# Kernel tuning notes

Hardware: AMD Instinct MI355X
Metric: run time of the kernel (lower is better)

Reference implementation:

```python
import jax, jax.numpy as jnp
import numpy as np

HEADS = 8
DIM_HEAD = 64
LN_EPS = 1e-5


def _layernorm(x, gamma, beta):
    mu = jnp.mean(x, axis=-1, keepdims=True)
    var = jnp.var(x, axis=-1, keepdims=True)
    return (x - mu) * jax.lax.rsqrt(var + LN_EPS) * gamma + beta


def setup_inputs() -> dict:
    key = jax.random.key(0)
    ks = jax.random.split(key, 5)
    B, N, D = 1, 16384, 512
    return {
        "x": jax.random.normal(ks[0], (B, N, D), dtype=jnp.float32),
        "ln_gamma": jnp.ones((D,), dtype=jnp.float32),
        "ln_beta": jnp.zeros((D,), dtype=jnp.float32),
        "w_qkv": jax.random.normal(ks[1], (D, 3 * D), dtype=jnp.float32) * (D ** -0.5),
        "agent": jax.random.normal(ks[2], (HEADS, 512, DIM_HEAD), dtype=jnp.float32) * (DIM_HEAD ** -0.5),
        "w_out": jax.random.normal(ks[3], (D, D), dtype=jnp.float32) * (D ** -0.5),
        "b_out": jnp.zeros((D,), dtype=jnp.float32),
    }


def reference(x, ln_gamma, ln_beta, w_qkv, agent, w_out, b_out):
    # TransLayer: x + Mask_Agent_Attention(LayerNorm(x))
    B, N, D = x.shape
    xn = _layernorm(x, ln_gamma, ln_beta)

    qkv = xn @ w_qkv                                   # [B, N, 3D]
    q, k, v = jnp.split(qkv, 3, axis=-1)
    # [B, H, N, d]
    q = q.reshape(B, N, HEADS, DIM_HEAD).transpose(0, 2, 1, 3)
    k = k.reshape(B, N, HEADS, DIM_HEAD).transpose(0, 2, 1, 3)
    v = v.reshape(B, N, HEADS, DIM_HEAD).transpose(0, 2, 1, 3)

    scale = DIM_HEAD ** -0.5  # tem=0 -> classical 1/sqrt(d) scaling

    # agents aggregate values: softmax over keys  [B, H, A, N]
    attn1 = jax.nn.softmax(jnp.einsum('had,bhnd->bhan', agent, k) * scale, axis=-1)
    agent_v = jnp.einsum('bhan,bhnd->bhad', attn1, v)  # [B, H, A, d]

    # queries attend to agents: softmax over agents  [B, H, N, A]
    attn2 = jax.nn.softmax(jnp.einsum('bhnd,had->bhna', q, agent) * scale, axis=-1)
    out = jnp.einsum('bhna,bhad->bhnd', attn2, agent_v)  # [B, H, N, d]

    out = out + v  # residual=True: value residual inside attention
    out = out.transpose(0, 2, 1, 3).reshape(B, N, D)
    out = out @ w_out + b_out
    return x + out
```

## Files before the change

### kernel.cpp

```cpp
#include <hip/hip_runtime.h>
#include <stdint.h>

typedef unsigned short u16;
typedef __attribute__((ext_vector_type(8))) short bf16x8;
typedef __attribute__((ext_vector_type(4))) float f32x4;

__device__ __forceinline__ float bf2f(u16 u){
  union { uint32_t i; float f; } v; v.i = ((uint32_t)u) << 16; return v.f;
}
__device__ __forceinline__ u16 f2bf(float f){
  union { float fl; uint32_t i; } v; v.fl = f;
  uint32_t r = v.i + 0x7FFFu + ((v.i >> 16) & 1u);
  return (u16)(r >> 16);
}
__device__ __forceinline__ f32x4 mfma16(bf16x8 a, bf16x8 b, f32x4 c){
  return __builtin_amdgcn_mfma_f32_16x16x32_bf16(a, b, c, 0, 0, 0);
}

__global__ __launch_bounds__(256) void k_conv_bf(const float* __restrict__ in, u16* __restrict__ out, int n){
  int i = (blockIdx.x * 256 + threadIdx.x) * 4;
  if (i >= n) return;
  float4 v = *(const float4*)(in + i);
  ushort4 o; o.x=f2bf(v.x); o.y=f2bf(v.y); o.z=f2bf(v.z); o.w=f2bf(v.w);
  *(ushort4*)(out + i) = o;
}

__global__ __launch_bounds__(256) void k_transp(const float* __restrict__ in, u16* __restrict__ out, int R, int C){
  __shared__ u16 tile[64][68];
  int c0 = blockIdx.x * 64, r0 = blockIdx.y * 64;
  int tr = threadIdx.x >> 4;
  int tc = (threadIdx.x & 15) * 4;
  for (int rr = 0; rr < 4; rr++){
    int r = rr * 16 + tr;
    float4 v = *(const float4*)(in + (size_t)(r0 + r) * C + c0 + tc);
    ushort4 o; o.x=f2bf(v.x); o.y=f2bf(v.y); o.z=f2bf(v.z); o.w=f2bf(v.w);
    *(ushort4*)&tile[r][tc] = o;
  }
  __syncthreads();
  for (int rr = 0; rr < 4; rr++){
    int oc = rr * 16 + tr;
    ushort4 o;
    o.x = tile[tc+0][oc]; o.y = tile[tc+1][oc]; o.z = tile[tc+2][oc]; o.w = tile[tc+3][oc];
    *(ushort4*)(out + (size_t)(c0 + oc) * R + r0 + tc) = o;
  }
}

__global__ __launch_bounds__(256) void k_transp_v(const u16* __restrict__ qkv, u16* __restrict__ vT){
  __shared__ u16 tile[64][68];
  int n0 = blockIdx.x * 64;
  int c0 = blockIdx.y * 64;
  int tr = threadIdx.x >> 4;
  int tc = (threadIdx.x & 15) * 4;
  for (int rr = 0; rr < 4; rr++){
    int r = rr * 16 + tr;
    ushort4 v = *(const ushort4*)(qkv + (size_t)(n0 + r) * 1536 + 1024 + c0 + tc);
    *(ushort4*)&tile[r][tc] = v;
  }
  __syncthreads();
  for (int rr = 0; rr < 4; rr++){
    int oc = rr * 16 + tr;
    ushort4 o;
    o.x = tile[tc+0][oc]; o.y = tile[tc+1][oc]; o.z = tile[tc+2][oc]; o.w = tile[tc+3][oc];
    *(ushort4*)(vT + (size_t)(c0 + oc) * 16384 + n0 + tc) = o;
  }
}

__global__ __launch_bounds__(128) void k_ln(const float* __restrict__ x, const float* __restrict__ g,
                                            const float* __restrict__ b, u16* __restrict__ xn){
  int row = blockIdx.x;
  int t = threadIdx.x;
  float4 v = *(const float4*)(x + (size_t)row * 512 + t * 4);
  float s = v.x + v.y + v.z + v.w;
  float q = v.x*v.x + v.y*v.y + v.z*v.z + v.w*v.w;
  for (int o = 32; o > 0; o >>= 1){ s += __shfl_down(s, o); q += __shfl_down(q, o); }
  __shared__ float red[4];
  if ((t & 63) == 0){ red[(t >> 6) * 2] = s; red[(t >> 6) * 2 + 1] = q; }
  __syncthreads();
  float mu  = (red[0] + red[2]) * (1.0f/512.0f);
  float var = (red[1] + red[3]) * (1.0f/512.0f) - mu * mu;
  float rs = rsqrtf(var + 1e-5f);
  float4 gv = *(const float4*)(g + t * 4);
  float4 bv = *(const float4*)(b + t * 4);
  ushort4 o;
  o.x = f2bf((v.x - mu) * rs * gv.x + bv.x);
  o.y = f2bf((v.y - mu) * rs * gv.y + bv.y);
  o.z = f2bf((v.z - mu) * rs * gv.z + bv.z);
  o.w = f2bf((v.w - mu) * rs * gv.w + bv.w);
  *(ushort4*)(xn + (size_t)row * 512 + t * 4) = o;
}

__global__ __launch_bounds__(256) void k_gemm_qkv(const u16* __restrict__ A, const u16* __restrict__ Bt,
                                                  u16* __restrict__ C){
  __shared__ u16 a_lds[128][72];
  __shared__ u16 b_lds[128][72];
  int m0 = blockIdx.x * 128, n0 = blockIdx.y * 128;
  int t = threadIdx.x, w = t >> 6, l = t & 63;
  int wm = (w >> 1) * 64, wn = (w & 1) * 64;
  f32x4 acc[4][4];
  for (int i=0;i<4;i++) for (int j=0;j<4;j++) acc[i][j] = {0.f,0.f,0.f,0.f};
  for (int k0 = 0; k0 < 512; k0 += 64){
    __syncthreads();
    for (int i = 0; i < 4; i++){
      int flat = t + 256 * i;
      int r = flat >> 3, c = (flat & 7) * 8;
      *(uint4*)&a_lds[r][c] = *(const uint4*)(A  + (size_t)(m0 + r) * 512 + k0 + c);
      *(uint4*)&b_lds[r][c] = *(const uint4*)(Bt + (size_t)(n0 + r) * 512 + k0 + c);
    }
    __syncthreads();
    for (int kk = 0; kk < 64; kk += 32){
      int kb = kk + (l >> 4) * 8;
      bf16x8 av[4], bv[4];
      for (int mt=0;mt<4;mt++) av[mt] = *(const bf16x8*)&a_lds[wm + mt*16 + (l & 15)][kb];
      for (int nt=0;nt<4;nt++) bv[nt] = *(const bf16x8*)&b_lds[wn + nt*16 + (l & 15)][kb];
      for (int mt=0;mt<4;mt++) for (int nt=0;nt<4;nt++)
        acc[mt][nt] = mfma16(av[mt], bv[nt], acc[mt][nt]);
    }
  }
  int rr = (l >> 4) * 4, cc = l & 15;
  for (int mt=0;mt<4;mt++) for (int nt=0;nt<4;nt++)
    for (int j=0;j<4;j++){
      int r = m0 + wm + mt*16 + rr + j;
      int c = n0 + wn + nt*16 + cc;
      C[(size_t)r * 1536 + c] = f2bf(acc[mt][nt][j]);
    }
}

__global__ __launch_bounds__(256) void k_gemm_out(const u16* __restrict__ A, const u16* __restrict__ Bt,
                                                  const float* __restrict__ x, const float* __restrict__ bias,
                                                  float* __restrict__ y){
  __shared__ u16 a_lds[128][72];
  __shared__ u16 b_lds[128][72];
  int m0 = blockIdx.x * 128, n0 = blockIdx.y * 128;
  int t = threadIdx.x, w = t >> 6, l = t & 63;
  int wm = (w >> 1) * 64, wn = (w & 1) * 64;
  f32x4 acc[4][4];
  for (int i=0;i<4;i++) for (int j=0;j<4;j++) acc[i][j] = {0.f,0.f,0.f,0.f};
  for (int k0 = 0; k0 < 512; k0 += 64){
    __syncthreads();
    for (int i = 0; i < 4; i++){
      int flat = t + 256 * i;
      int r = flat >> 3, c = (flat & 7) * 8;
      *(uint4*)&a_lds[r][c] = *(const uint4*)(A  + (size_t)(m0 + r) * 512 + k0 + c);
      *(uint4*)&b_lds[r][c] = *(const uint4*)(Bt + (size_t)(n0 + r) * 512 + k0 + c);
    }
    __syncthreads();
    for (int kk = 0; kk < 64; kk += 32){
      int kb = kk + (l >> 4) * 8;
      bf16x8 av[4], bv[4];
      for (int mt=0;mt<4;mt++) av[mt] = *(const bf16x8*)&a_lds[wm + mt*16 + (l & 15)][kb];
      for (int nt=0;nt<4;nt++) bv[nt] = *(const bf16x8*)&b_lds[wn + nt*16 + (l & 15)][kb];
      for (int mt=0;mt<4;mt++) for (int nt=0;nt<4;nt++)
        acc[mt][nt] = mfma16(av[mt], bv[nt], acc[mt][nt]);
    }
  }
  int rr = (l >> 4) * 4, cc = l & 15;
  for (int mt=0;mt<4;mt++) for (int nt=0;nt<4;nt++)
    for (int j=0;j<4;j++){
      int r = m0 + wm + mt*16 + rr + j;
      int c = n0 + wn + nt*16 + cc;
      y[(size_t)r * 512 + c] = acc[mt][nt][j] + bias[c] + x[(size_t)r * 512 + c];
    }
}

__global__ __launch_bounds__(256) void k_agent_agg(const u16* __restrict__ agbf, const u16* __restrict__ qkv,
                                                   const u16* __restrict__ vT,
                                                   float* __restrict__ nump, float* __restrict__ denp){
  int L = blockIdx.x;
  int g = (L >> 6) * 8 + (L & 7);
  int m = (L >> 3) & 7;
  int h = g >> 4, ch = g & 15, a0 = m * 64;

  __shared__ u16 ag[64][72];
  __shared__ u16 kt[64][72];
  __shared__ u16 vt[64][72];
  __shared__ u16 pt[64][72];
  int t = threadIdx.x, w = t >> 6, l = t & 63;

  for (int i = 0; i < 2; i++){
    int flat = t + 256 * i;
    int r = flat >> 3, c = (flat & 7) * 8;
    *(uint4*)&ag[r][c] = *(const uint4*)(agbf + (size_t)(h * 512 + a0 + r) * 64 + c);
  }

  bf16x8 ones;
  for (int i = 0; i < 8; i++) ones[i] = (short)0x3F80;

  f32x4 acc2[4];
  for (int i=0;i<4;i++) acc2[i] = {0.f,0.f,0.f,0.f};
  f32x4 accd = {0.f,0.f,0.f,0.f};

  for (int sub = 0; sub < 16; sub++){
    int n0 = ch * 1024 + sub * 64;
    __syncthreads();
    {
      int flat = t;
      int r = flat >> 3, c = (flat & 7) * 8;
      *(uint4*)&kt[r][c] = *(const uint4*)(qkv + (size_t)(n0 + r) * 1536 + 512 + h * 64 + c);
      int flat2 = t + 256;
      int r2 = flat2 >> 3, c2 = (flat2 & 7) * 8;
      *(uint4*)&kt[r2][c2] = *(const uint4*)(qkv + (size_t)(n0 + r2) * 1536 + 512 + h * 64 + c2);
      *(uint4*)&vt[r][c]   = *(const uint4*)(vT + ((size_t)(h * 64 + r) << 14) + n0 + c);
      *(uint4*)&vt[r2][c2] = *(const uint4*)(vT + ((size_t)(h * 64 + r2) << 14) + n0 + c2);
    }
    __syncthreads();

    f32x4 s[4];
    for (int nt=0;nt<4;nt++) s[nt] = {0.f,0.f,0.f,0.f};
    for (int kk = 0; kk < 64; kk += 32){
      int kb = kk + (l >> 4) * 8;
      bf16x8 kf = *(const bf16x8*)&kt[w*16 + (l & 15)][kb];
      for (int nt=0;nt<4;nt++){
        bf16x8 af = *(const bf16x8*)&ag[nt*16 + (l & 15)][kb];
        s[nt] = mfma16(kf, af, s[nt]);
      }
    }
    int nb = w*16 + (l >> 4) * 4;
    for (int nt=0;nt<4;nt++){
      int a = nt*16 + (l & 15);
      ushort4 o;
      o.x = f2bf(__expf(s[nt][0] * 0.125f));
      o.y = f2bf(__expf(s[nt][1] * 0.125f));
      o.z = f2bf(__expf(s[nt][2] * 0.125f));
      o.w = f2bf(__expf(s[nt][3] * 0.125f));
      *(ushort4*)&pt[a][nb] = o;
    }
    __syncthreads();

    for (int kk = 0; kk < 64; kk += 32){
      int kb = kk + (l >> 4) * 8;
      bf16x8 vf = *(const bf16x8*)&vt[w*16 + (l & 15)][kb];
      for (int mt=0;mt<4;mt++){
        bf16x8 pf = *(const bf16x8*)&pt[mt*16 + (l & 15)][kb];
        acc2[mt] = mfma16(pf, vf, acc2[mt]);
      }
      bf16x8 pw = *(const bf16x8*)&pt[w*16 + (l & 15)][kb];
      accd = mfma16(ones, pw, accd);
    }
  }

  size_t base = ((size_t)(h * 16 + ch) * 512 + a0) * 64;
  for (int mt=0;mt<4;mt++)
    #pragma unroll
    for (int j=0;j<4;j++){
      int a = mt*16 + (l>>4)*4 + j;
      int d = w*16 + (l&15);
      nump[base + (size_t)a*64 + d] = acc2[mt][j];
    }
  if (l < 16) denp[(size_t)(h*16 + ch) * 512 + a0 + w*16 + l] = accd[0];
}

__global__ __launch_bounds__(64) void k_agent_reduce(const float* __restrict__ nump, const float* __restrict__ denp,
                                                     u16* __restrict__ avtg){
  int h = blockIdx.x >> 9;
  int a = blockIdx.x & 511;
  int d = threadIdx.x;
  float num = 0.f, den = 0.f;
  for (int c = 0; c < 16; c++){
    num += nump[((size_t)(h * 16 + c) * 512 + a) * 64 + d];
    den += denp[(size_t)(h * 16 + c) * 512 + a];
  }
  avtg[((size_t)h * 64 + d) * 512 + a] = f2bf(num / den);
}

__global__ __launch_bounds__(256) void k_qattn(const u16* __restrict__ qkv, const u16* __restrict__ agbf,
                                               const u16* __restrict__ avtg, u16* __restrict__ atto){
  int n0 = blockIdx.x * 128;
  int h  = blockIdx.y;
  __shared__ u16 qt[128][72];
  __shared__ u16 avt[64][136];
  __shared__ u16 ubuf[128 * 136];
  __shared__ float dred[128][2];
  __shared__ float dnf[128];
  int t = threadIdx.x, w = t >> 6, l = t & 63;
  for (int i = 0; i < 4; i++){
    int flat = t + 256 * i;
    int r = flat >> 3, c = (flat & 7) * 8;
    *(uint4*)&qt[r][c] = *(const uint4*)(qkv + (size_t)(n0 + r) * 1536 + h * 64 + c);
  }
  f32x4 acc[4][2];
  for (int i=0;i<4;i++) for (int j=0;j<2;j++) acc[i][j] = {0.f,0.f,0.f,0.f};
  float dpart = 0.f;
  int wn = (w >> 1) * 64, wd = (w & 1) * 32, wa = (w & 1) * 64;
  for (int at = 0; at < 4; at++){
    int a0 = at * 128;
    __syncthreads();
    for (int i = 0; i < 4; i++){
      int flat = t + 256 * i;
      int r = flat >> 3, c = (flat & 7) * 8;
      *(uint4*)&ubuf[r * 72 + c] = *(const uint4*)(agbf + (size_t)(h * 512 + a0 + r) * 64 + c);
      int r2 = flat >> 4, c2 = (flat & 15) * 8;
      *(uint4*)&avt[r2][c2] = *(const uint4*)(avtg + (size_t)(h * 64 + r2) * 512 + a0 + c2);
    }
    __syncthreads();
    f32x4 s[4][4];
    for (int i=0;i<4;i++) for (int j=0;j<4;j++) s[i][j] = {0.f,0.f,0.f,0.f};
    for (int kk = 0; kk < 64; kk += 32){
      int kb = kk + (l >> 4) * 8;
      bf16x8 av[4], bv[4];
      for (int mt=0;mt<4;mt++) av[mt] = *(const bf16x8*)&qt[wn + mt*16 + (l&15)][kb];
      for (int nt=0;nt<4;nt++) bv[nt] = *(const bf16x8*)&ubuf[(size_t)(wa + nt*16 + (l&15)) * 72 + kb];
      for (int mt=0;mt<4;mt++) for (int nt=0;nt<4;nt++)
        s[mt][nt] = mfma16(av[mt], bv[nt], s[mt][nt]);
    }
    __syncthreads();
    for (int mt=0;mt<4;mt++) for (int nt=0;nt<4;nt++)
      #pragma unroll
      for (int j=0;j<4;j++){
        int n = wn + mt*16 + (l>>4)*4 + j;
        int a = wa + nt*16 + (l&15);
        ubuf[(size_t)n * 136 + a] = f2bf(__expf(s[mt][nt][j] * 0.125f));
      }
    __syncthreads();
    {
      const uint4* pp = (const uint4*)&ubuf[(size_t)(t >> 1) * 136 + (t & 1) * 64];
      float ds = 0.f;
      #pragma unroll
      for (int qq = 0; qq < 8; qq++){
        uint4 u = pp[qq];
        const u16* us = (const u16*)&u;
        for (int j=0;j<8;j++) ds += bf2f(us[j]);
      }
      dpart += ds;
    }
    for (int kk = 0; kk < 128; kk += 32){
      int kb = kk + (l >> 4) * 8;
      bf16x8 bv[2];
      for (int nt=0;nt<2;nt++) bv[nt] = *(const bf16x8*)&avt[wd + nt*16 + (l&15)][kb];
      for (int mt=0;mt<4;mt++){
        bf16x8 av = *(const bf16x8*)&ubuf[(size_t)(wn + mt*16 + (l&15)) * 136 + kb];
        for (int nt=0;nt<2;nt++)
          acc[mt][nt] = mfma16(av, bv[nt], acc[mt][nt]);
      }
    }
  }
  dred[t >> 1][t & 1] = dpart;
  __syncthreads();
  if (t < 128) dnf[t] = dred[t][0] + dred[t][1];
  __syncthreads();
  for (int mt=0;mt<4;mt++) for (int nt=0;nt<2;nt++)
    #pragma unroll
    for (int j=0;j<4;j++){
      int n = wn + mt*16 + (l>>4)*4 + j;
      int d = wd + nt*16 + (l&15);
      float v = bf2f(qkv[(size_t)(n0 + n) * 1536 + 1024 + h * 64 + d]);
      atto[(size_t)(n0 + n) * 512 + h * 64 + d] = f2bf(acc[mt][nt][j] / dnf[n] + v);
    }
}

extern "C" void kernel_launch(void* const* d_in, const int* in_sizes, int n_in,
                              void* d_out, int out_size, void* d_ws, size_t ws_size,
                              hipStream_t stream) {
  const float* x     = (const float*)d_in[0];
  const float* gamma = (const float*)d_in[1];
  const float* beta  = (const float*)d_in[2];
  const float* w_qkv = (const float*)d_in[3];
  const float* agent = (const float*)d_in[4];
  const float* w_out = (const float*)d_in[5];
  const float* b_out = (const float*)d_in[6];
  float* y = (float*)d_out;

  char* ws = (char*)d_ws;
  u16*   xn    = (u16*)  (ws + 0);
  u16*   vT    = (u16*)  (ws + 0);
  u16*   qkv   = (u16*)  (ws + 16777216);
  u16*   wqkvt = (u16*)  (ws + 67108864);
  u16*   woutt = (u16*)  (ws + 68681728);
  u16*   agbf  = (u16*)  (ws + 69206016);
  u16*   avtg  = (u16*)  (ws + 69730304);
  u16*   atto  = (u16*)  (ws + 70254592);
  float* nump  = (float*)(ws + 87031808);
  float* denp  = (float*)(ws + 103809024);

  k_conv_bf   <<<dim3(256),     dim3(256), 0, stream>>>(agent, agbf, 8*512*64);
  k_transp    <<<dim3(24, 8),   dim3(256), 0, stream>>>(w_qkv, wqkvt, 512, 1536);
  k_transp    <<<dim3(8, 8),    dim3(256), 0, stream>>>(w_out, woutt, 512, 512);
  k_ln        <<<dim3(16384),   dim3(128), 0, stream>>>(x, gamma, beta, xn);
  k_gemm_qkv  <<<dim3(128, 12), dim3(256), 0, stream>>>(xn, wqkvt, qkv);
  k_transp_v  <<<dim3(256, 8),  dim3(256), 0, stream>>>(qkv, vT);
  k_agent_agg <<<dim3(1024),    dim3(256), 0, stream>>>(agbf, qkv, vT, nump, denp);
  k_agent_reduce<<<dim3(4096),  dim3(64),  0, stream>>>(nump, denp, avtg);
  k_qattn     <<<dim3(128, 8),  dim3(256), 0, stream>>>(qkv, agbf, avtg, atto);
  k_gemm_out  <<<dim3(128, 4),  dim3(256), 0, stream>>>(atto, woutt, x, b_out, y);
}
```

Before: 187.4 us.

## Fold softmax scale into agents, use exp2, restructure query-attention tiling

Pre-scales the agent matrix by scale*log2(e) at conversion time so both softmax stages can use the hardware exp2 with no per-element multiply, and packs bf16 conversions with v_cvt_pk_bf16_f32. The query-attention kernel moves to 64-row tiles over 8 agent chunks of 64, twice as many blocks, and a smaller LDS footprint. It computes the row denominator with an MFMA against a ones vector instead of a scalar LDS reduction, and multiplies by a reciprocal instead of dividing. This trades some MFMA work and more synchronisation steps for higher occupancy and fewer scalar ops.

Result: faster. 171.0 us (-8.7%).

```diff
diff --git a/kernel.cpp b/kernel.cpp
--- a/kernel.cpp
+++ b/kernel.cpp
@@ -13,15 +13,20 @@
   uint32_t r = v.i + 0x7FFFu + ((v.i >> 16) & 1u);
   return (u16)(r >> 16);
 }
+__device__ __forceinline__ uint32_t cvt_pk_bf16(float lo, float hi){
+  uint32_t r;
+  asm("v_cvt_pk_bf16_f32 %0, %1, %2" : "=v"(r) : "v"(lo), "v"(hi));
+  return r;
+}
 __device__ __forceinline__ f32x4 mfma16(bf16x8 a, bf16x8 b, f32x4 c){
   return __builtin_amdgcn_mfma_f32_16x16x32_bf16(a, b, c, 0, 0, 0);
 }
 
-__global__ __launch_bounds__(256) void k_conv_bf(const float* __restrict__ in, u16* __restrict__ out, int n){
+__global__ __launch_bounds__(256) void k_conv_bf(const float* __restrict__ in, u16* __restrict__ out, int n, float scale){
   int i = (blockIdx.x * 256 + threadIdx.x) * 4;
   if (i >= n) return;
   float4 v = *(const float4*)(in + i);
-  ushort4 o; o.x=f2bf(v.x); o.y=f2bf(v.y); o.z=f2bf(v.z); o.w=f2bf(v.w);
+  ushort4 o; o.x=f2bf(v.x*scale); o.y=f2bf(v.y*scale); o.z=f2bf(v.z*scale); o.w=f2bf(v.w*scale);
   *(ushort4*)(out + i) = o;
 }
 
@@ -217,12 +222,10 @@
     int nb = w*16 + (l >> 4) * 4;
     for (int nt=0;nt<4;nt++){
       int a = nt*16 + (l & 15);
-      ushort4 o;
-      o.x = f2bf(__expf(s[nt][0] * 0.125f));
-      o.y = f2bf(__expf(s[nt][1] * 0.125f));
-      o.z = f2bf(__expf(s[nt][2] * 0.125f));
-      o.w = f2bf(__expf(s[nt][3] * 0.125f));
-      *(ushort4*)&pt[a][nb] = o;
+      uint32_t w0 = cvt_pk_bf16(__builtin_amdgcn_exp2f(s[nt][0]), __builtin_amdgcn_exp2f(s[nt][1]));
+      uint32_t w1 = cvt_pk_bf16(__builtin_amdgcn_exp2f(s[nt][2]), __builtin_amdgcn_exp2f(s[nt][3]));
+      uint2 o; o.x = w0; o.y = w1;
+      *(uint2*)&pt[a][nb] = o;
     }
     __syncthreads();
 
@@ -264,87 +267,85 @@
 
 __global__ __launch_bounds__(256) void k_qattn(const u16* __restrict__ qkv, const u16* __restrict__ agbf,
                                                const u16* __restrict__ avtg, u16* __restrict__ atto){
-  int n0 = blockIdx.x * 128;
+  int n0 = blockIdx.x * 64;
   int h  = blockIdx.y;
-  __shared__ u16 qt[128][72];
-  __shared__ u16 avt[64][136];
-  __shared__ u16 ubuf[128 * 136];
-  __shared__ float dred[128][2];
-  __shared__ float dnf[128];
+  __shared__ u16 qt[64][72];
+  __shared__ u16 ag[64][72];
+  __shared__ u16 avt[64][72];
+  __shared__ u16 pt[64][72];
+  __shared__ float dnf[64];
   int t = threadIdx.x, w = t >> 6, l = t & 63;
-  for (int i = 0; i < 4; i++){
+
+  for (int i = 0; i < 2; i++){
     int flat = t + 256 * i;
     int r = flat >> 3, c = (flat & 7) * 8;
     *(uint4*)&qt[r][c] = *(const uint4*)(qkv + (size_t)(n0 + r) * 1536 + h * 64 + c);
   }
-  f32x4 acc[4][2];
-  for (int i=0;i<4;i++) for (int j=0;j<2;j++) acc[i][j] = {0.f,0.f,0.f,0.f};
-  float dpart = 0.f;
-  int wn = (w >> 1) * 64, wd = (w & 1) * 32, wa = (w & 1) * 64;
-  for (int at = 0; at < 4; at++){
-    int a0 = at * 128;
-    __syncthreads();
-    for (int i = 0; i < 4; i++){
+
+  bf16x8 ones;
+  for (int i = 0; i < 8; i++) ones[i] = (short)0x3F80;
+
+  f32x4 acc[4];
+  for (int i=0;i<4;i++) acc[i] = {0.f,0.f,0.f,0.f};
+  f32x4 accd = {0.f,0.f,0.f,0.f};
+
+  for (int at = 0; at < 8; at++){
+    int a0 = at * 64;
+    __syncthreads();
+    for (int i = 0; i < 2; i++){
       int flat = t + 256 * i;
       int r = flat >> 3, c = (flat & 7) * 8;
-      *(uint4*)&ubuf[r * 72 + c] = *(const uint4*)(agbf + (size_t)(h * 512 + a0 + r) * 64 + c);
-      int r2 = flat >> 4, c2 = (flat & 15) * 8;
-      *(uint4*)&avt[r2][c2] = *(const uint4*)(avtg + (size_t)(h * 64 + r2) * 512 + a0 + c2);
-    }
-    __syncthreads();
-    f32x4 s[4][4];
-    for (int i=0;i<4;i++) for (int j=0;j<4;j++) s[i][j] = {0.f,0.f,0.f,0.f};
-    for (int kk = 0; kk < 64; kk += 32){
-      int kb = kk + (l >> 4) * 8;
-      bf16x8 av[4], bv[4];
-      for (int mt=0;mt<4;mt++) av[mt] = *(const bf16x8*)&qt[wn + mt*16 + (l&15)][kb];
-      for (int nt=0;nt<4;nt++) bv[nt] = *(const bf16x8*)&ubuf[(size_t)(wa + nt*16 + (l&15)) * 72 + kb];
-      for (int mt=0;mt<4;mt++) for (int nt=0;nt<4;nt++)
-        s[mt][nt] = mfma16(av[mt], bv[nt], s[mt][nt]);
-    }
-    __syncthreads();
-    for (int mt=0;mt<4;mt++) for (int nt=0;nt<4;nt++)
-      #pragma unroll
-      for (int j=0;j<4;j++){
-        int n = wn + mt*16 + (l>>4)*4 + j;
-        int a = wa + nt*16 + (l&15);
-        ubuf[(size_t)n * 136 + a] = f2bf(__expf(s[mt][nt][j] * 0.125f));
+      *(uint4*)&ag[r][c]  = *(const uint4*)(agbf + (size_t)(h * 512 + a0 + r) * 64 + c);
+      *(uint4*)&avt[r][c] = *(const uint4*)(avtg + (size_t)(h * 64 + r) * 512 + a0 + c);
+    }
+    __syncthreads();
+
+    f32x4 s[4];
+    for (int nt=0;nt<4;nt++) s[nt] = {0.f,0.f,0.f,0.f};
+    for (int kk = 0; kk < 64; kk += 32){
+      int kb = kk + (l >> 4) * 8;
+      bf16x8 af = *(const bf16x8*)&ag[w*16 + (l & 15)][kb];
+      for (int nt=0;nt<4;nt++){
+        bf16x8 qf = *(const bf16x8*)&qt[nt*16 + (l & 15)][kb];
+        s[nt] = mfma16(af, qf, s[nt]);
       }
-    __syncthreads();
-    {
-      const uint4* pp = (const uint4*)&ubuf[(size_t)(t >> 1) * 136 + (t & 1) * 64];
-      float ds = 0.f;
-      #pragma unroll
-      for (int qq = 0; qq < 8; qq++){
-        uint4 u = pp[qq];
-        const u16* us = (const u16*)&u;
-        for (int j=0;j<8;j++) ds += bf2f(us[j]);
+    }
+    int ab = w*16 + (l >> 4) * 4;
+    for (int nt=0;nt<4;nt++){
+      int n = nt*16 + (l & 15);
+      uint32_t w0 = cvt_pk_bf16(__builtin_amdgcn_exp2f(s[nt][0]), __builtin_amdgcn_exp2f(s[nt][1]));
+      uint32_t w1 = cvt_pk_bf16(__builtin_amdgcn_exp2f(s[nt][2]), __builtin_amdgcn_exp2f(s[nt][3]));
+      uint2 o; o.x = w0; o.y = w1;
+      *(uint2*)&pt[n][ab] = o;
+    }
+    __syncthreads();
+
+    for (int kk = 0; kk < 64; kk += 32){
+      int kb = kk + (l >> 4) * 8;
+      bf16x8 vf = *(const bf16x8*)&avt[w*16 + (l & 15)][kb];
+      for (int mt=0;mt<4;mt++){
+        bf16x8 pf = *(const bf16x8*)&pt[mt*16 + (l & 15)][kb];
+        acc[mt] = mfma16(pf, vf, acc[mt]);
       }
-      dpart += ds;
-    }
-    for (int kk = 0; kk < 128; kk += 32){
-      int kb = kk + (l >> 4) * 8;
-      bf16x8 bv[2];
-      for (int nt=0;nt<2;nt++) bv[nt] = *(const bf16x8*)&avt[wd + nt*16 + (l&15)][kb];
-      for (int mt=0;mt<4;mt++){
-        bf16x8 av = *(const bf16x8*)&ubuf[(size_t)(wn + mt*16 + (l&15)) * 136 + kb];
-        for (int nt=0;nt<2;nt++)
-          acc[mt][nt] = mfma16(av, bv[nt], acc[mt][nt]);
-      }
-    }
-  }
-  dred[t >> 1][t & 1] = dpart;
-  __syncthreads();
-  if (t < 128) dnf[t] = dred[t][0] + dred[t][1];
-  __syncthreads();
-  for (int mt=0;mt<4;mt++) for (int nt=0;nt<2;nt++)
+      bf16x8 pw = *(const bf16x8*)&pt[w*16 + (l & 15)][kb];
+      accd = mfma16(ones, pw, accd);
+    }
+  }
+
+  if (l < 16) dnf[w*16 + l] = accd[0];
+  __syncthreads();
+  if (t < 64) dnf[t] = __builtin_amdgcn_rcpf(dnf[t]);
+  __syncthreads();
+
+  int d = w*16 + (l & 15);
+  for (int mt=0;mt<4;mt++){
     #pragma unroll
     for (int j=0;j<4;j++){
-      int n = wn + mt*16 + (l>>4)*4 + j;
-      int d = wd + nt*16 + (l&15);
+      int n = mt*16 + (l>>4)*4 + j;
       float v = bf2f(qkv[(size_t)(n0 + n) * 1536 + 1024 + h * 64 + d]);
-      atto[(size_t)(n0 + n) * 512 + h * 64 + d] = f2bf(acc[mt][nt][j] / dnf[n] + v);
-    }
+      atto[(size_t)(n0 + n) * 512 + h * 64 + d] = f2bf(acc[mt][j] * dnf[n] + v);
+    }
+  }
 }
 
 extern "C" void kernel_launch(void* const* d_in, const int* in_sizes, int n_in,
@@ -371,7 +372,7 @@
   float* nump  = (float*)(ws + 87031808);
   float* denp  = (float*)(ws + 103809024);
 
-  k_conv_bf   <<<dim3(256),     dim3(256), 0, stream>>>(agent, agbf, 8*512*64);
+  k_conv_bf   <<<dim3(256),     dim3(256), 0, stream>>>(agent, agbf, 8*512*64, 0.125f * 1.44269504089f);
   k_transp    <<<dim3(24, 8),   dim3(256), 0, stream>>>(w_qkv, wqkvt, 512, 1536);
   k_transp    <<<dim3(8, 8),    dim3(256), 0, stream>>>(w_out, woutt, 512, 512);
   k_ln        <<<dim3(16384),   dim3(128), 0, stream>>>(x, gamma, beta, xn);
@@ -379,6 +380,6 @@
   k_transp_v  <<<dim3(256, 8),  dim3(256), 0, stream>>>(qkv, vT);
   k_agent_agg <<<dim3(1024),    dim3(256), 0, stream>>>(agbf, qkv, vT, nump, denp);
   k_agent_reduce<<<dim3(4096),  dim3(64),  0, stream>>>(nump, denp, avtg);
-  k_qattn     <<<dim3(128, 8),  dim3(256), 0, stream>>>(qkv, agbf, avtg, atto);
+  k_qattn     <<<dim3(256, 8),  dim3(256), 0, stream>>>(qkv, agbf, avtg, atto);
   k_gemm_out  <<<dim3(128, 4),  dim3(256), 0, stream>>>(atto, woutt, x, b_out, y);
 }
```
